# Kernel optimization log

Measured on AMD Instinct MI355X. Metric: run time of the kernel, lower is better.

## Reference

```python
import jax, jax.numpy as jnp
import numpy as np

# Dims from HierarchicalDecoder defaults; NB is the torch batch size, which the
# original code accidentally uses as the LSTM time axis (2D input to nn.LSTM).
Z_DIM, U, COND, HID, OUT, NB = 512, 16, 512, 1024, 16, 512


def _unif(key, shape, scale):
    return jax.random.uniform(key, shape, jnp.float32, -scale, scale)


def setup_inputs() -> dict:
    key = jax.random.key(0)
    ks = jax.random.split(key, 20)
    d = Z_DIM // U            # 32
    sd = 1.0 / np.sqrt(d)
    sc = 1.0 / np.sqrt(COND)
    sh = 1.0 / np.sqrt(HID)
    return {
        "z": jax.random.normal(ks[0], (NB, Z_DIM), jnp.float32),
        "fc0_w": _unif(ks[1], (COND, d), sd), "fc0_b": _unif(ks[2], (COND,), sd),
        "fc1_w": _unif(ks[3], (HID, COND), sc), "fc1_b": _unif(ks[4], (HID,), sc),
        # conductor LSTM (2 layers, input=hidden=COND); b = b_ih + b_hh fused
        "c_wih0": _unif(ks[5], (4 * COND, COND), sc), "c_whh0": _unif(ks[6], (4 * COND, COND), sc), "c_b0": _unif(ks[7], (4 * COND,), sc),
        "c_wih1": _unif(ks[8], (4 * COND, COND), sc), "c_whh1": _unif(ks[9], (4 * COND, COND), sc), "c_b1": _unif(ks[10], (4 * COND,), sc),
        # decoder LSTM (2 layers, input COND->HID then HID->HID)
        "d_wih0": _unif(ks[11], (4 * HID, COND), sh), "d_whh0": _unif(ks[12], (4 * HID, HID), sh), "d_b0": _unif(ks[13], (4 * HID,), sh),
        "d_wih1": _unif(ks[14], (4 * HID, HID), sh), "d_whh1": _unif(ks[15], (4 * HID, HID), sh), "d_b1": _unif(ks[16], (4 * HID,), sh),
        "out_w": _unif(ks[17], (OUT, HID), sh), "out_b": _unif(ks[18], (OUT,), sh),
    }


def _lstm_layer(x, h0, c0, wih, whh, b):
    # x: [U, T, I]; h0, c0: [U, H]. PyTorch gate order: i, f, g, o.
    gx = jnp.einsum('uti,gi->utg', x, wih) + b  # input contribution, hoisted out of scan

    def step(carry, g):
        h, c = carry
        g = g + h @ whh.T
        i, f, gg, o = jnp.split(g, 4, axis=-1)
        c = jax.nn.sigmoid(f) * c + jax.nn.sigmoid(i) * jnp.tanh(gg)
        h = jax.nn.sigmoid(o) * jnp.tanh(c)
        return (h, c), h

    (hT, _), hs = jax.lax.scan(step, (h0, c0), jnp.swapaxes(gx, 0, 1))
    return jnp.swapaxes(hs, 0, 1), hT  # [U, T, H], [U, H]


def _forward(z, fc0_w, fc0_b, fc1_w, fc1_b, c_wih0, c_whh0, c_b0, c_wih1, c_whh1, c_b1,
             d_wih0, d_whh0, d_b0, d_wih1, d_whh1, d_b1, out_w, out_b):
    B = z.shape[0]
    # [U, B, z_dim//U]; the Python loop over U in the original is vectorized as a batch axis.
    x = jnp.swapaxes(z.reshape(B, U, -1), 0, 1)
    x = jnp.tanh(x @ fc0_w.T + fc0_b)  # fc0 -> [U, B, COND]; B is the LSTM time axis
    zC = jnp.zeros((U, COND), x.dtype)
    h0s, hT0 = _lstm_layer(x, zC, zC, c_wih0, c_whh0, c_b0)
    h1s, hT1 = _lstm_layer(h0s, zC, zC, c_wih1, c_whh1, c_b1)
    # fc1 on final conductor hidden of each layer -> decoder initial h; initial c = 0
    hd0 = jnp.tanh(hT0 @ fc1_w.T + fc1_b)
    hd1 = jnp.tanh(hT1 @ fc1_w.T + fc1_b)
    zH = jnp.zeros((U, HID), x.dtype)
    d0s, _ = _lstm_layer(h1s, hd0, zH, d_wih0, d_whh0, d_b0)
    d1s, _ = _lstm_layer(d0s, hd1, zH, d_wih1, d_whh1, d_b1)
    logits = d1s @ out_w.T + out_b                 # [U, B, OUT]
    probs = jax.nn.softmax(logits, axis=1)         # Softmax(dim=0) over the B axis per subsequence
    return jnp.swapaxes(probs, 0, 1).reshape(B, U * OUT)  # torch.cat(outputs, dim=1)


def reference(z, fc0_w, fc0_b, fc1_w, fc1_b, c_wih0, c_whh0, c_b0, c_wih1, c_whh1, c_b1,
              d_wih0, d_whh0, d_b0, d_wih1, d_whh1, d_b1, out_w, out_b):
    return _forward(z, fc0_w, fc0_b, fc1_w, fc1_b, c_wih0, c_whh0, c_b0, c_wih1, c_whh1, c_b1,
                    d_wih0, d_whh0, d_b0, d_wih1, d_whh1, d_b1, out_w, out_b)
```

## Files before the change

kernel.cpp:

```cpp
#include <hip/hip_runtime.h>
#include <hip/hip_bf16.h>
#include <cstdio>


typedef __attribute__((ext_vector_type(8))) short short8;
typedef __attribute__((ext_vector_type(4))) float f32x4;
using bf16 = __hip_bfloat16;

__device__ __forceinline__ float bfraw2f(short s){
  return __uint_as_float(((unsigned)(unsigned short)s) << 16);
}

__device__ __forceinline__ void gbar_arrive(unsigned* cnt){
  asm volatile("s_waitcnt vmcnt(0)" ::: "memory");
  __syncthreads();
  if (threadIdx.x == 0)
    __hip_atomic_fetch_add(&cnt[(blockIdx.x & 15) * 32], 1u,
                           __ATOMIC_RELAXED, __HIP_MEMORY_SCOPE_AGENT);
}
__device__ __forceinline__ void gbar_wait(const unsigned* cnt, unsigned target){
  if (threadIdx.x < 64){
    const int l = threadIdx.x;
    for (;;){
      bool ok = true;
      if (l < 16)
        ok = __hip_atomic_load(&cnt[l * 32], __ATOMIC_RELAXED,
                               __HIP_MEMORY_SCOPE_AGENT) >= target;
      if (__all(ok)) break;
      __builtin_amdgcn_s_sleep(1);
    }
    __builtin_amdgcn_fence(__ATOMIC_ACQUIRE, "agent");
  }
  __syncthreads();
}

template<int N>
__device__ __forceinline__ void ldA(const bf16* base, short8* av){
#pragma unroll
  for (int i = 0; i < N; ++i)
    av[i] = *(const short8*)(base + i * 32);
}

__device__ __forceinline__ void st2_sc1(bf16* p, unsigned v){
  asm volatile("global_store_short %0, %1, off sc0 sc1" :: "v"(p), "v"(v) : "memory");
}

__device__ __forceinline__ void gates_store(const float v[4], float* c_st, int g,
                                            int kg, int j, bf16* hrow, int Hl,
                                            float* hTp)
{
#pragma unroll
  for (int rr = 0; rr < 4; ++rr){
    float a = (g == 2) ? tanhf(v[rr]) : 1.f / (1.f + expf(-v[rr]));
    float x1 = __shfl_xor(a, 1);
    float x2 = __shfl_xor(a, 2);
    float x3 = __shfl_xor(x1, 2);
    float cn = x1 * c_st[rr] + a * x2;
    float hn = x3 * tanhf(cn);
    c_st[rr] = cn;
    if (g == 0){
      int u = kg * 4 + rr;
      bf16 hb = __float2bfloat16(hn);
      unsigned us = *reinterpret_cast<unsigned short*>(&hb);
      st2_sc1(hrow + (size_t)u * Hl + j, us);
      if (hTp) hTp[(size_t)u * Hl + j] = hn;
    }
  }
}

__global__ void k_prep_w(const float* __restrict__ srcA, const float* __restrict__ srcB,
                         int K1, int K2, int H, bf16* __restrict__ dst)
{
  const int row = blockIdx.x;
  const int j = row >> 2, g = row & 3;
  const int Kt = K1 + K2;
  const float* sA = srcA + (size_t)(g * H + j) * K1;
  const float* sB = srcB ? srcB + (size_t)(g * H + j) * K2 : nullptr;
  bf16* d = dst + (size_t)row * Kt;
  for (int k = threadIdx.x; k < Kt; k += blockDim.x)
    d[k] = __float2bfloat16(k < K1 ? sA[k] : sB[k - K1]);
}

__global__ void k_prep_b(const float* __restrict__ src, int H, float* __restrict__ dst){
  int i = blockIdx.x * blockDim.x + threadIdx.x;
  if (i < 4 * H) dst[i] = src[(i & 3) * H + (i >> 2)];
}

__global__ void k_conv_bf(const float* __restrict__ src, bf16* __restrict__ dst, int n){
  int i = blockIdx.x * blockDim.x + threadIdx.x;
  if (i < n) dst[i] = __float2bfloat16(src[i]);
}

__global__ void k_fc0(const float* __restrict__ z, const float* __restrict__ w,
                      const float* __restrict__ b, bf16* __restrict__ x)
{
  const int m = blockIdx.x;
  const int t = m >> 4, u = m & 15;
  const float* zr = z + (size_t)t * 512 + u * 32;
  float zv[32];
#pragma unroll
  for (int k = 0; k < 32; ++k) zv[k] = zr[k];
  for (int n = threadIdx.x; n < 512; n += 256){
    const float* wr = w + n * 32;
    float s = b[n];
#pragma unroll
    for (int k = 0; k < 32; ++k) s += zv[k] * wr[k];
    x[(size_t)m * 512 + n] = __float2bfloat16(tanhf(s));
  }
}

__device__ __forceinline__ void gload16(const void* g, void* lds_wave_base){
  __builtin_amdgcn_global_load_lds((const __attribute__((address_space(1))) void*)g,
                                   (__attribute__((address_space(3))) void*)lds_wave_base,
                                   16, 0, 0);
}

__global__ __launch_bounds__(256) void k_gemm_gx0(const bf16* __restrict__ A,
                                                  const bf16* __restrict__ W,
                                                  const float* __restrict__ bias,
                                                  float* __restrict__ C)
{
  __shared__ bf16 Al[128 * 64];
  __shared__ bf16 Bl[128 * 64];
  const int tid = threadIdx.x, lane = tid & 63, wave = tid >> 6;
  const int bm = blockIdx.x & 63, bn = blockIdx.x >> 6;
  const int wm = wave >> 1, wn = wave & 1;
  const int col = lane & 15, kg = lane >> 4;

  f32x4 acc[4][4];
#pragma unroll
  for (int i = 0; i < 4; ++i)
#pragma unroll
    for (int q = 0; q < 4; ++q) acc[i][q] = f32x4{0.f, 0.f, 0.f, 0.f};

  const int r = tid >> 3, c8 = (tid & 7) * 8;
  for (int k0 = 0; k0 < 512; k0 += 64){
    const bf16* ga = A + (size_t)(bm * 128 + r) * 512 + k0 + c8;
    const bf16* gb = W + (size_t)(bn * 128 + r) * 512 + k0 + c8;
#pragma unroll
    for (int i = 0; i < 4; ++i){
      gload16(ga + (size_t)32 * i * 512, (char*)Al + (size_t)i * 4096 + wave * 1024);
      gload16(gb + (size_t)32 * i * 512, (char*)Bl + (size_t)i * 4096 + wave * 1024);
    }
    __syncthreads();
#pragma unroll
    for (int kb = 0; kb < 2; ++kb){
      short8 af[4], bfr[4];
#pragma unroll
      for (int i = 0; i < 4; ++i)
        af[i] = *(const short8*)&Al[(wm * 64 + i * 16 + col) * 64 + kb * 32 + kg * 8];
#pragma unroll
      for (int i = 0; i < 4; ++i)
        bfr[i] = *(const short8*)&Bl[(wn * 64 + i * 16 + col) * 64 + kb * 32 + kg * 8];
#pragma unroll
      for (int i = 0; i < 4; ++i)
#pragma unroll
        for (int q = 0; q < 4; ++q)
          acc[i][q] = __builtin_amdgcn_mfma_f32_16x16x32_bf16(af[i], bfr[q], acc[i][q], 0, 0, 0);
    }
    __syncthreads();
  }
#pragma unroll
  for (int i = 0; i < 4; ++i)
#pragma unroll
    for (int q = 0; q < 4; ++q){
      int cc = bn * 128 + wn * 64 + q * 16 + col;
      float bv = bias[cc];
#pragma unroll
      for (int rr = 0; rr < 4; ++rr){
        int rrow = bm * 128 + wm * 64 + i * 16 + kg * 4 + rr;
        C[(size_t)rrow * 2048 + cc] = acc[i][q][rr] + bv;
      }
    }
}

__global__ __launch_bounds__(512, 2) void k_cond(
    const bf16* __restrict__ Wc0, const bf16* __restrict__ Wc1,
    const float* __restrict__ bc1, const float* __restrict__ gx0,
    bf16* h0seq, bf16* h1seq, float* hT0, float* hT1, unsigned* cnt)
{
  const int wg = blockIdx.x, tid = threadIdx.x;
  const int lane = tid & 63, wave = tid >> 6;
  const int col = lane & 15, kg = lane >> 4;
  const int r = col;
  const bool L0 = wg < 16;
  __shared__ f32x4 part[4][64];

  int tileIdx, half = 0;
  if (L0) tileIdx = wg * 8 + wave;
  else  { tileIdx = (wg - 16) * 4 + (wave >> 1); half = wave & 1; }
  const int colp = tileIdx * 16 + col;
  const int j = colp >> 2, g = colp & 3;

  short8 breg[16];
  {
    const bf16* W = L0 ? (Wc0 + (size_t)colp * 512)
                       : (Wc1 + (size_t)colp * 1024 + half * 512);
#pragma unroll
    for (int i = 0; i < 16; ++i) breg[i] = *(const short8*)(W + i * 32 + kg * 8);
  }
#pragma unroll
  for (int i = 0; i < 16; ++i) asm volatile("" : "+v"(breg[i]));

  const float bias = L0 ? 0.f : bc1[colp];
  float c_st[4] = {0.f, 0.f, 0.f, 0.f};
  float gxv[4];
  if (L0){
#pragma unroll
    for (int rr = 0; rr < 4; ++rr)
      gxv[rr] = gx0[((size_t)(kg * 4 + rr)) * 2048 + colp];
  }

  for (int tick = 0; tick < 513; ++tick){
    const int t = tick - (L0 ? 0 : 1);
    const bool active = (t >= 0 && t < 512);
    f32x4 acc = {0.f, 0.f, 0.f, 0.f};
    if (active){
      short8 av[16];
      const bf16* base;
      if (L0)             base = h0seq + (size_t)t * 16 * 512 + r * 512 + kg * 8;
      else if (half == 0) base = h0seq + (size_t)(t + 1) * 16 * 512 + r * 512 + kg * 8;
      else                base = h1seq + (size_t)t * 16 * 512 + r * 512 + kg * 8;
      ldA<16>(base, av);
      asm volatile("s_waitcnt vmcnt(0)" ::: "memory");
      __builtin_amdgcn_sched_barrier(0);
#pragma unroll
      for (int i = 0; i < 16; ++i)
        acc = __builtin_amdgcn_mfma_f32_16x16x32_bf16(av[i], breg[i], acc, 0, 0, 0);
      if (!L0 && half == 1) part[wave >> 1][lane] = acc;
    }
    if (!L0) __syncthreads();
    if (active && (L0 || half == 0)){
      float v[4];
      if (L0){
#pragma unroll
        for (int rr = 0; rr < 4; ++rr) v[rr] = acc[rr] + gxv[rr];
      } else {
        f32x4 p2 = part[wave >> 1][lane];
#pragma unroll
        for (int rr = 0; rr < 4; ++rr) v[rr] = acc[rr] + p2[rr] + bias;
      }
      bf16* hrow = (L0 ? h0seq : h1seq) + (size_t)(t + 1) * 16 * 512;
      float* hTp = (t == 511) ? (L0 ? hT0 : hT1) : nullptr;
      gates_store(v, c_st, g, kg, j, hrow, 512, hTp);
    }
    gbar_arrive(cnt);
    if (L0 && tick + 1 < 512){
#pragma unroll
      for (int rr = 0; rr < 4; ++rr)
        gxv[rr] = gx0[((size_t)(tick + 1) * 16 + kg * 4 + rr) * 2048 + colp];
    }
    gbar_wait(cnt, 3u * (tick + 1));
  }
}

__global__ void k_hd(const float* __restrict__ hT0, const float* __restrict__ hT1,
                     const float* __restrict__ w, const float* __restrict__ b,
                     bf16* __restrict__ d0s0, bf16* __restrict__ d1s0)
{
  int gid = blockIdx.x * 256 + threadIdx.x;
  int sel = gid >> 14;
  int u = (gid >> 10) & 15, n = gid & 1023;
  const float* h = (sel ? hT1 : hT0) + u * 512;
  const float* wr = w + (size_t)n * 512;
  float s = b[n];
  for (int k = 0; k < 512; ++k) s += h[k] * wr[k];
  (sel ? d1s0 : d0s0)[(size_t)u * 1024 + n] = __float2bfloat16(tanhf(s));
}

__global__ __launch_bounds__(512, 2) void k_dec(
    const bf16* __restrict__ Wd0, const bf16* __restrict__ Wd1,
    const float* __restrict__ bd0, const float* __restrict__ bd1,
    const bf16* __restrict__ h1seq, bf16* d0seq, bf16* d1seq, unsigned* cnt)
{
  const int wg = blockIdx.x, tid = threadIdx.x;
  const int lane = tid & 63, wave = tid >> 6;
  const int col = lane & 15, kg = lane >> 4, r = col;
  const bool L0 = wg < 128;
  const int grp = wave >> 2, q = wave & 3;
  const int tileIdx = (L0 ? wg : wg - 128) * 2 + grp;
  const int colp = tileIdx * 16 + col;
  const int j = colp >> 2, g = colp & 3;
  __shared__ f32x4 part[2][3][64];

  short8 breg[16];
#pragma unroll
  for (int i = 0; i < 16; ++i) breg[i] = short8{0,0,0,0,0,0,0,0};
  if (L0){
    const bf16* W = Wd0 + (size_t)colp * 1536 + q * 384;
#pragma unroll
    for (int i = 0; i < 12; ++i) breg[i] = *(const short8*)(W + i * 32 + kg * 8);
  } else {
    const bf16* W = Wd1 + (size_t)colp * 2048 + q * 512;
#pragma unroll
    for (int i = 0; i < 16; ++i) breg[i] = *(const short8*)(W + i * 32 + kg * 8);
  }
#pragma unroll
  for (int i = 0; i < 16; ++i) asm volatile("" : "+v"(breg[i]));

  const float bias = L0 ? bd0[colp] : bd1[colp];
  float c_st[4] = {0.f, 0.f, 0.f, 0.f};

  for (int tick = 0; tick < 513; ++tick){
    const int t = tick - (L0 ? 0 : 1);
    const bool active = (t >= 0 && t < 512);
    f32x4 acc = {0.f, 0.f, 0.f, 0.f};
    if (active){
      short8 av[16];
      if (L0){
        const bf16* h1p = h1seq + (size_t)(t + 1) * 16 * 512 + r * 512 + kg * 8;
        const bf16* d0p = d0seq + (size_t)t * 16 * 1024 + r * 1024 + kg * 8;
        if      (q == 0)  ldA<12>(h1p, av);
        else if (q == 1){ ldA<4>(h1p + 384, av); ldA<8>(d0p, av + 4); }
        else if (q == 2)  ldA<12>(d0p + 256, av);
        else              ldA<12>(d0p + 640, av);
      } else {
        const bf16* d0n = d0seq + (size_t)(t + 1) * 16 * 1024 + r * 1024 + kg * 8;
        const bf16* d1c = d1seq + (size_t)t * 16 * 1024 + r * 1024 + kg * 8;
        if      (q == 0) ldA<16>(d0n, av);
        else if (q == 1) ldA<16>(d0n + 512, av);
        else if (q == 2) ldA<16>(d1c, av);
        else             ldA<16>(d1c + 512, av);
      }
      asm volatile("s_waitcnt vmcnt(0)" ::: "memory");
      __builtin_amdgcn_sched_barrier(0);
      if (L0){
#pragma unroll
        for (int i = 0; i < 12; ++i)
          acc = __builtin_amdgcn_mfma_f32_16x16x32_bf16(av[i], breg[i], acc, 0, 0, 0);
      } else {
#pragma unroll
        for (int i = 0; i < 16; ++i)
          acc = __builtin_amdgcn_mfma_f32_16x16x32_bf16(av[i], breg[i], acc, 0, 0, 0);
      }
      if (q != 0) part[grp][q - 1][lane] = acc;
    }
    __syncthreads();
    if (active && q == 0){
      f32x4 p0 = part[grp][0][lane], p1 = part[grp][1][lane], p2 = part[grp][2][lane];
      float v[4];
#pragma unroll
      for (int rr = 0; rr < 4; ++rr) v[rr] = acc[rr] + p0[rr] + p1[rr] + p2[rr] + bias;
      bf16* hrow = (L0 ? d0seq : d1seq) + (size_t)(t + 1) * 16 * 1024;
      gates_store(v, c_st, g, kg, j, hrow, 1024, nullptr);
    }
    gbar_arrive(cnt);
    gbar_wait(cnt, 16u * (tick + 1));
  }
}

__global__ __launch_bounds__(256) void k_logits(const bf16* __restrict__ d1seq,
                                                const bf16* __restrict__ ow,
                                                const float* __restrict__ ob,
                                                float* __restrict__ logits)
{
  const int u = blockIdx.x >> 4, tb = blockIdx.x & 15;
  __shared__ bf16 rows[32][1024];
  const int tid = threadIdx.x;
  for (int idx = tid; idx < 4096; idx += 256){
    int tl = idx >> 7, seg = idx & 127;
    *(short8*)&rows[tl][seg * 8] =
      *(const short8*)(d1seq + ((size_t)(tb * 32 + tl + 1) * 16 + u) * 1024 + seg * 8);
  }
  __syncthreads();
  for (int p = tid; p < 512; p += 256){
    int tl = p >> 4, o = p & 15;
    const bf16* wr = ow + (size_t)o * 1024;
    float s = 0.f;
    for (int k = 0; k < 1024; k += 8){
      short8 av = *(const short8*)&rows[tl][k];
      short8 wv = *(const short8*)(wr + k);
#pragma unroll
      for (int e = 0; e < 8; ++e) s += bfraw2f(av[e]) * bfraw2f(wv[e]);
    }
    logits[((size_t)u * 16 + o) * 512 + tb * 32 + tl] = s + ob[o];
  }
}

__global__ __launch_bounds__(256) void k_softmax(const float* __restrict__ logits,
                                                 float* __restrict__ out)
{
  const int u = blockIdx.x >> 4, o = blockIdx.x & 15;
  const float* L = logits + ((size_t)u * 16 + o) * 512;
  const int tid = threadIdx.x;
  float v0 = L[tid], v1 = L[tid + 256];
  float m = fmaxf(v0, v1);
  for (int d = 1; d < 64; d <<= 1) m = fmaxf(m, __shfl_xor(m, d));
  __shared__ float red[4], red2[4];
  if ((tid & 63) == 0) red[tid >> 6] = m;
  __syncthreads();
  m = fmaxf(fmaxf(red[0], red[1]), fmaxf(red[2], red[3]));
  float e0 = expf(v0 - m), e1 = expf(v1 - m);
  float s = e0 + e1;
  for (int d = 1; d < 64; d <<= 1) s += __shfl_xor(s, d);
  if ((tid & 63) == 0) red2[tid >> 6] = s;
  __syncthreads();
  s = red2[0] + red2[1] + red2[2] + red2[3];
  float inv = 1.f / s;
  out[(size_t)tid * 256 + u * 16 + o] = e0 * inv;
  out[(size_t)(tid + 256) * 256 + u * 16 + o] = e1 * inv;
}

extern "C" void kernel_launch(void* const* d_in, const int* in_sizes, int n_in,
                              void* d_out, int out_size, void* d_ws, size_t ws_size,
                              hipStream_t stream)
{
  const float* z      = (const float*)d_in[0];
  const float* fc0_w  = (const float*)d_in[1];
  const float* fc0_b  = (const float*)d_in[2];
  const float* fc1_w  = (const float*)d_in[3];
  const float* fc1_b  = (const float*)d_in[4];
  const float* c_wih0 = (const float*)d_in[5];
  const float* c_whh0 = (const float*)d_in[6];
  const float* c_b0   = (const float*)d_in[7];
  const float* c_wih1 = (const float*)d_in[8];
  const float* c_whh1 = (const float*)d_in[9];
  const float* c_b1   = (const float*)d_in[10];
  const float* d_wih0 = (const float*)d_in[11];
  const float* d_whh0 = (const float*)d_in[12];
  const float* d_b0   = (const float*)d_in[13];
  const float* d_wih1 = (const float*)d_in[14];
  const float* d_whh1 = (const float*)d_in[15];
  const float* d_b1   = (const float*)d_in[16];
  const float* out_w  = (const float*)d_in[17];
  const float* out_b  = (const float*)d_in[18];

  char* p = (char*)d_ws;
  auto alloc = [&](size_t bytes) -> char* {
    char* r = p; p += (bytes + 255) & ~(size_t)255; return r;
  };
  bf16*  Wgx0p  = (bf16*)alloc(2048ull * 512 * 2);
  bf16*  Wc0p   = (bf16*)alloc(2048ull * 512 * 2);
  bf16*  Wc1p   = (bf16*)alloc(2048ull * 1024 * 2);
  bf16*  Wd0p   = (bf16*)alloc(4096ull * 1536 * 2);
  bf16*  Wd1p   = (bf16*)alloc(4096ull * 2048 * 2);
  float* bc0p   = (float*)alloc(2048 * 4);
  float* bc1p   = (float*)alloc(2048 * 4);
  float* bd0p   = (float*)alloc(4096 * 4);
  float* bd1p   = (float*)alloc(4096 * 4);
  bf16*  outwbf = (bf16*)alloc(16384 * 2);
  bf16*  x      = (bf16*)alloc(8192ull * 512 * 2);
  float* gx0    = (float*)alloc(8192ull * 2048 * 4);
  bf16*  h0seq  = (bf16*)alloc(513ull * 16 * 512 * 2);
  bf16*  h1seq  = (bf16*)alloc(513ull * 16 * 512 * 2);
  bf16*  d0seq  = (bf16*)alloc(513ull * 16 * 1024 * 2);
  bf16*  d1seq  = (bf16*)alloc(513ull * 16 * 1024 * 2);
  float* hT0    = (float*)alloc(16 * 512 * 4);
  float* hT1    = (float*)alloc(16 * 512 * 4);
  float* logits = (float*)alloc(16ull * 16 * 512 * 4);
  unsigned* cntC = (unsigned*)alloc(16 * 32 * 4);
  unsigned* cntD = (unsigned*)alloc(16 * 32 * 4);
  if ((size_t)(p - (char*)d_ws) > ws_size){
    fprintf(stderr, "kernel_launch: ws too small (%zu needed, %zu given)\n",
            (size_t)(p - (char*)d_ws), ws_size);
    return;
  }

  hipMemsetAsync(cntC, 0, 16 * 32 * 4, stream);
  hipMemsetAsync(cntD, 0, 16 * 32 * 4, stream);
  hipMemsetAsync(h0seq, 0, 16 * 512 * 2, stream);
  hipMemsetAsync(h1seq, 0, 16 * 512 * 2, stream);

  k_prep_w<<<2048, 256, 0, stream>>>(c_wih0, nullptr, 512, 0,   512, Wgx0p);
  k_prep_w<<<2048, 256, 0, stream>>>(c_whh0, nullptr, 512, 0,   512, Wc0p);
  k_prep_w<<<2048, 256, 0, stream>>>(c_wih1, c_whh1, 512, 512,  512, Wc1p);
  k_prep_w<<<4096, 256, 0, stream>>>(d_wih0, d_whh0, 512, 1024, 1024, Wd0p);
  k_prep_w<<<4096, 256, 0, stream>>>(d_wih1, d_whh1, 1024, 1024, 1024, Wd1p);
  k_prep_b<<<8,  256, 0, stream>>>(c_b0, 512,  bc0p);
  k_prep_b<<<8,  256, 0, stream>>>(c_b1, 512,  bc1p);
  k_prep_b<<<16, 256, 0, stream>>>(d_b0, 1024, bd0p);
  k_prep_b<<<16, 256, 0, stream>>>(d_b1, 1024, bd1p);
  k_conv_bf<<<64, 256, 0, stream>>>(out_w, outwbf, 16 * 1024);

  k_fc0<<<8192, 256, 0, stream>>>(z, fc0_w, fc0_b, x);
  k_gemm_gx0<<<1024, 256, 0, stream>>>(x, Wgx0p, bc0p, gx0);

  k_cond<<<48, 512, 0, stream>>>(Wc0p, Wc1p, bc1p, gx0, h0seq, h1seq, hT0, hT1, cntC);
  k_hd<<<128, 256, 0, stream>>>(hT0, hT1, fc1_w, fc1_b, d0seq, d1seq);
  k_dec<<<256, 512, 0, stream>>>(Wd0p, Wd1p, bd0p, bd1p, h1seq, d0seq, d1seq, cntD);

  k_logits<<<256, 256, 0, stream>>>(d1seq, outwbf, out_b, logits);
  k_softmax<<<256, 256, 0, stream>>>(logits, (float*)d_out);
}
```

Baseline: 8.449 ms.

## Replace atomic-counter grid barrier with per-block flags and pack hidden-state stores

The grid barrier in the persistent LSTM kernels is changed from atomic fetch-add on 16 padded counters to per-workgroup generation flags written with plain atomic stores. A single wave polls all flags, 48 for the conductor and 256 for the decoder. Per-block stores remove contention on the shared counters but make each poll read more locations. The gate epilogue also gathers four adjacent hidden units by lane shuffles, so one lane writes them with a single packed 8-byte store instead of four 2-byte stores, reducing store count on the per-step critical path.

```diff
diff --git a/kernel.cpp b/kernel.cpp
--- a/kernel.cpp
+++ b/kernel.cpp
@@ -5,27 +5,38 @@
 
 typedef __attribute__((ext_vector_type(8))) short short8;
 typedef __attribute__((ext_vector_type(4))) float f32x4;
+typedef __attribute__((ext_vector_type(2))) unsigned int u32x2;
 using bf16 = __hip_bfloat16;
 
 __device__ __forceinline__ float bfraw2f(short s){
   return __uint_as_float(((unsigned)(unsigned short)s) << 16);
 }
-
-__device__ __forceinline__ void gbar_arrive(unsigned* cnt){
+__device__ __forceinline__ unsigned bfbits(float f){
+  __hip_bfloat16 h = __float2bfloat16(f);
+  return (unsigned)*reinterpret_cast<unsigned short*>(&h);
+}
+
+__device__ __forceinline__ void gbar_arrive(unsigned* flags, unsigned gen){
   asm volatile("s_waitcnt vmcnt(0)" ::: "memory");
   __syncthreads();
   if (threadIdx.x == 0)
-    __hip_atomic_fetch_add(&cnt[(blockIdx.x & 15) * 32], 1u,
-                           __ATOMIC_RELAXED, __HIP_MEMORY_SCOPE_AGENT);
-}
-__device__ __forceinline__ void gbar_wait(const unsigned* cnt, unsigned target){
+    __hip_atomic_store(&flags[blockIdx.x], gen,
+                       __ATOMIC_RELAXED, __HIP_MEMORY_SCOPE_AGENT);
+}
+template<int NWG>
+__device__ __forceinline__ void gbar_wait(const unsigned* flags, unsigned gen){
   if (threadIdx.x < 64){
     const int l = threadIdx.x;
+    constexpr int R = (NWG + 63) / 64;
     for (;;){
       bool ok = true;
-      if (l < 16)
-        ok = __hip_atomic_load(&cnt[l * 32], __ATOMIC_RELAXED,
-                               __HIP_MEMORY_SCOPE_AGENT) >= target;
+#pragma unroll
+      for (int k = 0; k < R; ++k){
+        int idx = l + k * 64;
+        if (idx < NWG)
+          ok &= (__hip_atomic_load(&flags[idx], __ATOMIC_RELAXED,
+                                   __HIP_MEMORY_SCOPE_AGENT) >= gen);
+      }
       if (__all(ok)) break;
       __builtin_amdgcn_s_sleep(1);
     }
@@ -40,15 +51,16 @@
   for (int i = 0; i < N; ++i)
     av[i] = *(const short8*)(base + i * 32);
 }
-
-__device__ __forceinline__ void st2_sc1(bf16* p, unsigned v){
-  asm volatile("global_store_short %0, %1, off sc0 sc1" :: "v"(p), "v"(v) : "memory");
-}
-
-__device__ __forceinline__ void gates_store(const float v[4], float* c_st, int g,
-                                            int kg, int j, bf16* hrow, int Hl,
-                                            float* hTp)
-{
+__device__ __forceinline__ void vm0(){
+  asm volatile("s_waitcnt vmcnt(0)" ::: "memory");
+  __builtin_amdgcn_sched_barrier(0);
+}
+
+__device__ __forceinline__ void gate_tile(const float v[4], float* c_st,
+                                          int col, int kg, int jb,
+                                          bf16* hrow, int Hl, float* hTrow)
+{
+  const int g = col & 3;
 #pragma unroll
   for (int rr = 0; rr < 4; ++rr){
     float a = (g == 2) ? tanhf(v[rr]) : 1.f / (1.f + expf(-v[rr]));
@@ -58,12 +70,19 @@
     float cn = x1 * c_st[rr] + a * x2;
     float hn = x3 * tanhf(cn);
     c_st[rr] = cn;
-    if (g == 0){
+    float h4 = __shfl_xor(hn, 4), h8 = __shfl_xor(hn, 8), h12 = __shfl_xor(hn, 12);
+    if (col == 0){
       int u = kg * 4 + rr;
-      bf16 hb = __float2bfloat16(hn);
-      unsigned us = *reinterpret_cast<unsigned short*>(&hb);
-      st2_sc1(hrow + (size_t)u * Hl + j, us);
-      if (hTp) hTp[(size_t)u * Hl + j] = hn;
+      u32x2 pk;
+      pk.x = bfbits(hn) | (bfbits(h4) << 16);
+      pk.y = bfbits(h8) | (bfbits(h12) << 16);
+      bf16* p = hrow + (size_t)u * Hl + jb;
+      asm volatile("global_store_dwordx2 %0, %1, off sc0 sc1"
+                   :: "v"(p), "v"(pk) : "memory");
+      if (hTrow){
+        f32x4 hv = {hn, h4, h8, h12};
+        *(f32x4*)(hTrow + (size_t)u * Hl + jb) = hv;
+      }
     }
   }
 }
@@ -177,7 +196,7 @@
 __global__ __launch_bounds__(512, 2) void k_cond(
     const bf16* __restrict__ Wc0, const bf16* __restrict__ Wc1,
     const float* __restrict__ bc1, const float* __restrict__ gx0,
-    bf16* h0seq, bf16* h1seq, float* hT0, float* hT1, unsigned* cnt)
+    bf16* h0seq, bf16* h1seq, float* hT0, float* hT1, unsigned* flags)
 {
   const int wg = blockIdx.x, tid = threadIdx.x;
   const int lane = tid & 63, wave = tid >> 6;
@@ -190,7 +209,7 @@
   if (L0) tileIdx = wg * 8 + wave;
   else  { tileIdx = (wg - 16) * 4 + (wave >> 1); half = wave & 1; }
   const int colp = tileIdx * 16 + col;
-  const int j = colp >> 2, g = colp & 3;
+  const int jb = tileIdx * 4;
 
   short8 breg[16];
   {
@@ -218,12 +237,11 @@
     if (active){
       short8 av[16];
       const bf16* base;
-      if (L0)             base = h0seq + (size_t)t * 16 * 512 + r * 512 + kg * 8;
-      else if (half == 0) base = h0seq + (size_t)(t + 1) * 16 * 512 + r * 512 + kg * 8;
-      else                base = h1seq + (size_t)t * 16 * 512 + r * 512 + kg * 8;
+      if (L0)             base = h0seq + (size_t)t * 8192 + r * 512 + kg * 8;
+      else if (half == 0) base = h0seq + (size_t)(t + 1) * 8192 + r * 512 + kg * 8;
+      else                base = h1seq + (size_t)t * 8192 + r * 512 + kg * 8;
       ldA<16>(base, av);
-      asm volatile("s_waitcnt vmcnt(0)" ::: "memory");
-      __builtin_amdgcn_sched_barrier(0);
+      vm0();
 #pragma unroll
       for (int i = 0; i < 16; ++i)
         acc = __builtin_amdgcn_mfma_f32_16x16x32_bf16(av[i], breg[i], acc, 0, 0, 0);
@@ -240,17 +258,17 @@
 #pragma unroll
         for (int rr = 0; rr < 4; ++rr) v[rr] = acc[rr] + p2[rr] + bias;
       }
-      bf16* hrow = (L0 ? h0seq : h1seq) + (size_t)(t + 1) * 16 * 512;
+      bf16* hrow = (L0 ? h0seq : h1seq) + (size_t)(t + 1) * 8192;
       float* hTp = (t == 511) ? (L0 ? hT0 : hT1) : nullptr;
-      gates_store(v, c_st, g, kg, j, hrow, 512, hTp);
-    }
-    gbar_arrive(cnt);
+      gate_tile(v, c_st, col, kg, jb, hrow, 512, hTp);
+    }
+    gbar_arrive(flags, (unsigned)(tick + 1));
     if (L0 && tick + 1 < 512){
 #pragma unroll
       for (int rr = 0; rr < 4; ++rr)
         gxv[rr] = gx0[((size_t)(tick + 1) * 16 + kg * 4 + rr) * 2048 + colp];
     }
-    gbar_wait(cnt, 3u * (tick + 1));
+    gbar_wait<48>(flags, (unsigned)(tick + 1));
   }
 }
 
@@ -271,7 +289,7 @@
 __global__ __launch_bounds__(512, 2) void k_dec(
     const bf16* __restrict__ Wd0, const bf16* __restrict__ Wd1,
     const float* __restrict__ bd0, const float* __restrict__ bd1,
-    const bf16* __restrict__ h1seq, bf16* d0seq, bf16* d1seq, unsigned* cnt)
+    const bf16* __restrict__ h1seq, bf16* d0seq, bf16* d1seq, unsigned* flags)
 {
   const int wg = blockIdx.x, tid = threadIdx.x;
   const int lane = tid & 63, wave = tid >> 6;
@@ -280,7 +298,7 @@
   const int grp = wave >> 2, q = wave & 3;
   const int tileIdx = (L0 ? wg : wg - 128) * 2 + grp;
   const int colp = tileIdx * 16 + col;
-  const int j = colp >> 2, g = colp & 3;
+  const int jb = tileIdx * 4;
   __shared__ f32x4 part[2][3][64];
 
   short8 breg[16];
@@ -308,22 +326,21 @@
     if (active){
       short8 av[16];
       if (L0){
-        const bf16* h1p = h1seq + (size_t)(t + 1) * 16 * 512 + r * 512 + kg * 8;
-        const bf16* d0p = d0seq + (size_t)t * 16 * 1024 + r * 1024 + kg * 8;
+        const bf16* h1p = h1seq + (size_t)(t + 1) * 8192 + r * 512 + kg * 8;
+        const bf16* d0p = d0seq + (size_t)t * 16384 + r * 1024 + kg * 8;
         if      (q == 0)  ldA<12>(h1p, av);
         else if (q == 1){ ldA<4>(h1p + 384, av); ldA<8>(d0p, av + 4); }
         else if (q == 2)  ldA<12>(d0p + 256, av);
         else              ldA<12>(d0p + 640, av);
       } else {
-        const bf16* d0n = d0seq + (size_t)(t + 1) * 16 * 1024 + r * 1024 + kg * 8;
-        const bf16* d1c = d1seq + (size_t)t * 16 * 1024 + r * 1024 + kg * 8;
+        const bf16* d0n = d0seq + (size_t)(t + 1) * 16384 + r * 1024 + kg * 8;
+        const bf16* d1c = d1seq + (size_t)t * 16384 + r * 1024 + kg * 8;
         if      (q == 0) ldA<16>(d0n, av);
         else if (q == 1) ldA<16>(d0n + 512, av);
         else if (q == 2) ldA<16>(d1c, av);
         else             ldA<16>(d1c + 512, av);
       }
-      asm volatile("s_waitcnt vmcnt(0)" ::: "memory");
-      __builtin_amdgcn_sched_barrier(0);
+      vm0();
       if (L0){
 #pragma unroll
         for (int i = 0; i < 12; ++i)
@@ -341,11 +358,11 @@
       float v[4];
 #pragma unroll
       for (int rr = 0; rr < 4; ++rr) v[rr] = acc[rr] + p0[rr] + p1[rr] + p2[rr] + bias;
-      bf16* hrow = (L0 ? d0seq : d1seq) + (size_t)(t + 1) * 16 * 1024;
-      gates_store(v, c_st, g, kg, j, hrow, 1024, nullptr);
-    }
-    gbar_arrive(cnt);
-    gbar_wait(cnt, 16u * (tick + 1));
+      bf16* hrow = (L0 ? d0seq : d1seq) + (size_t)(t + 1) * 16384;
+      gate_tile(v, c_st, col, kg, jb, hrow, 1024, nullptr);
+    }
+    gbar_arrive(flags, (unsigned)(tick + 1));
+    gbar_wait<256>(flags, (unsigned)(tick + 1));
   }
 }
 
@@ -448,16 +465,16 @@
   float* hT0    = (float*)alloc(16 * 512 * 4);
   float* hT1    = (float*)alloc(16 * 512 * 4);
   float* logits = (float*)alloc(16ull * 16 * 512 * 4);
-  unsigned* cntC = (unsigned*)alloc(16 * 32 * 4);
-  unsigned* cntD = (unsigned*)alloc(16 * 32 * 4);
+  unsigned* flagC = (unsigned*)alloc(64 * 4);
+  unsigned* flagD = (unsigned*)alloc(256 * 4);
   if ((size_t)(p - (char*)d_ws) > ws_size){
     fprintf(stderr, "kernel_launch: ws too small (%zu needed, %zu given)\n",
             (size_t)(p - (char*)d_ws), ws_size);
     return;
   }
 
-  hipMemsetAsync(cntC, 0, 16 * 32 * 4, stream);
-  hipMemsetAsync(cntD, 0, 16 * 32 * 4, stream);
+  hipMemsetAsync(flagC, 0, 64 * 4, stream);
+  hipMemsetAsync(flagD, 0, 256 * 4, stream);
   hipMemsetAsync(h0seq, 0, 16 * 512 * 2, stream);
   hipMemsetAsync(h1seq, 0, 16 * 512 * 2, stream);
 
@@ -475,9 +492,9 @@
   k_fc0<<<8192, 256, 0, stream>>>(z, fc0_w, fc0_b, x);
   k_gemm_gx0<<<1024, 256, 0, stream>>>(x, Wgx0p, bc0p, gx0);
 
-  k_cond<<<48, 512, 0, stream>>>(Wc0p, Wc1p, bc1p, gx0, h0seq, h1seq, hT0, hT1, cntC);
+  k_cond<<<48, 512, 0, stream>>>(Wc0p, Wc1p, bc1p, gx0, h0seq, h1seq, hT0, hT1, flagC);
   k_hd<<<128, 256, 0, stream>>>(hT0, hT1, fc1_w, fc1_b, d0seq, d1seq);
-  k_dec<<<256, 512, 0, stream>>>(Wd0p, Wd1p, bd0p, bd1p, h1seq, d0seq, d1seq, cntD);
+  k_dec<<<256, 512, 0, stream>>>(Wd0p, Wd1p, bd0p, bd1p, h1seq, d0seq, d1seq, flagD);
 
   k_logits<<<256, 256, 0, stream>>>(d1seq, outwbf, out_b, logits);
   k_softmax<<<256, 256, 0, stream>>>(logits, (float*)d_out);
```

Result: slower. 9.913 ms (+17.3%).
